# Kernel optimization log

Hardware: AMD Instinct MI355X
Metric: run time of the kernel (lower is better)

The kernel has to match this reference:

```python
import jax, jax.numpy as jnp
import numpy as np

N, E, F_IN, H, HEADS, L, DEPTH = 10000, 160000, 128, 64, 8, 6, 3
M = HEADS * H  # 512, fractal transform width
OUT_DIM = 64
EPS = 1e-5
CHAOS = 0.1


def _ln(x, g, b):
    mu = x.mean(-1, keepdims=True)
    var = x.var(-1, keepdims=True)
    return (x - mu) / jnp.sqrt(var + EPS) * g + b


def _ln_plain(x):
    mu = x.mean(-1, keepdims=True)
    var = x.var(-1, keepdims=True)
    return (x - mu) / jnp.sqrt(var + EPS)


def setup_inputs() -> dict:
    key = jax.random.key(0)
    ks = iter(jax.random.split(key, 64))
    r = lambda *s: jax.random.normal(next(ks), s, jnp.float32) * 0.05
    return dict(
        x=jax.random.normal(next(ks), (N, F_IN), jnp.float32),
        edge_index=jax.random.randint(next(ks), (2, E), 0, N),
        enc_W=r(F_IN, H), enc_b=jnp.zeros((H,)), enc_g=jnp.ones((H,)), enc_beta=jnp.zeros((H,)),
        chaos_memory=r(1, H),
        tW0=r(L, H, M), tb0=jnp.zeros((L, M)), tg0=jnp.ones((L, M)), tbeta0=jnp.zeros((L, M)),
        tW1=r(L, M, M), tb1=jnp.zeros((L, M)), tg1=jnp.ones((L, M)), tbeta1=jnp.zeros((L, M)),
        tW2=r(L, M, M), tb2=jnp.zeros((L, M)), tg2=jnp.ones((L, M)), tbeta2=jnp.zeros((L, M)),
        att=r(L, HEADS, 2 * H),
        evo_W1=r(H, 2 * H), evo_b1=jnp.zeros((2 * H,)),
        evo_W2=r(2 * H, H), evo_b2=jnp.zeros((H,)),
        dec_state_W=r(H, 1), dec_state_b=jnp.zeros((1,)),
        dec_imp_W=r(H, 1), dec_imp_b=jnp.zeros((1,)),
        dec_chaos_W=r(H, 1), dec_chaos_b=jnp.zeros((1,)),
        dec_evo_W=r(H, OUT_DIM), dec_evo_b=jnp.zeros((OUT_DIM,)),
    )


def reference(x, edge_index, enc_W, enc_b, enc_g, enc_beta, chaos_memory,
              tW0, tb0, tg0, tbeta0, tW1, tb1, tg1, tbeta1, tW2, tb2, tg2, tbeta2,
              att, evo_W1, evo_b1, evo_W2, evo_b2,
              dec_state_W, dec_state_b, dec_imp_W, dec_imp_b,
              dec_chaos_W, dec_chaos_b, dec_evo_W, dec_evo_b):
    src, dst = edge_index[0], edge_index[1]  # j -> i, aggregate at dst
    nkey = jax.random.key(42)

    # encoder (dropout inactive in eval)
    h = jax.nn.relu(_ln(x @ enc_W + enc_b, enc_g, enc_beta))
    h = h + chaos_memory * CHAOS  # [1,H] broadcast

    residuals = []
    for i in range(L):
        cf = CHAOS * (1.0 + 0.1 * i)
        h_prev = h
        # fractal transform stack: pre-noise features are averaged
        Ws = [(tW0[i], tb0[i], tg0[i], tbeta0[i]),
              (tW1[i], tb1[i], tg1[i], tbeta1[i]),
              (tW2[i], tb2[i], tg2[i], tbeta2[i])]
        cur = h
        feats = 0.0
        for d, (W, b, g, be) in enumerate(Ws):
            cur = jax.nn.relu(_ln(cur @ W + b, g, be))
            feats = feats + cur
            noise = jax.random.normal(jax.random.fold_in(nkey, i * 10 + d), cur.shape, cur.dtype)
            cur = cur + noise * cf  # chaotic perturbation feeds next depth only
        hm = (feats / DEPTH).reshape(-1, HEADS, H)  # [N, heads, out]
        # GAT-style edge attention: alpha_e = <[x_i||x_j], att>
        a_i = jnp.einsum('nhc,hc->nh', hm, att[i][:, :H])
        a_j = jnp.einsum('nhc,hc->nh', hm, att[i][:, H:])
        alpha = jax.nn.leaky_relu(a_i[dst] + a_j[src], 0.2)  # [E, heads]
        # segment softmax over incoming edges of each dst node
        amax = jax.ops.segment_max(alpha, dst, num_segments=N)
        ex = jnp.exp(alpha - amax[dst])
        denom = jax.ops.segment_sum(ex, dst, num_segments=N)
        w = ex / denom[dst]  # [E, heads]
        msg = hm[src] * w[:, :, None]  # [E, heads, out]
        agg = jax.ops.segment_sum(msg, dst, num_segments=N)  # [N, heads, out]
        h_new = agg.mean(axis=1)  # head-mean -> [N, H]
        gate = jax.nn.sigmoid(jnp.tanh(jax.nn.relu(h_new @ evo_W1 + evo_b1) @ evo_W2 + evo_b2))
        h = gate * h_new + (1.0 - gate) * h_prev
        residuals.append(h)
        h = _ln_plain(h)  # F.layer_norm without affine
    h_multi = sum(residuals) / L
    # batch is None -> decoders applied per-node on h_multi
    state = h_multi @ dec_state_W + dec_state_b
    importance = h_multi @ dec_imp_W + dec_imp_b
    chaos = h_multi @ dec_chaos_W + dec_chaos_b
    evolution = h_multi @ dec_evo_W + dec_evo_b
    return state, importance, chaos, evolution, h_multi
```

## Files before the change

### kernel.cpp

```cpp
#include <hip/hip_runtime.h>
#include <cstdint>
#include <cstddef>

#define NN 10000
#define EE 160000
#define F_IN 128
#define HH 64
#define HEADS 8
#define LL 6
#define MM 512
#define OUT_DIM 64
#define EPSF 1e-5f
#define ROWS 16
#define NB 625

typedef unsigned short ushort;
typedef __attribute__((ext_vector_type(8))) short bf16x8;
typedef __attribute__((ext_vector_type(8))) unsigned short ushort8;
typedef __attribute__((ext_vector_type(4))) float f32x4;

union U8 { ushort8 u; bf16x8 b; };

struct U2 { uint32_t a, b; };

__host__ __device__ constexpr uint32_t rotl32(uint32_t x, uint32_t d) {
  return (x << d) | (x >> (32u - d));
}

__host__ __device__ constexpr U2 threefry2x32(uint32_t k1, uint32_t k2, uint32_t x0, uint32_t x1) {
  uint32_t ks2 = k1 ^ k2 ^ 0x1BD11BDAu;
  x0 += k1; x1 += k2;
  x0 += x1; x1 = rotl32(x1, 13); x1 ^= x0;
  x0 += x1; x1 = rotl32(x1, 15); x1 ^= x0;
  x0 += x1; x1 = rotl32(x1, 26); x1 ^= x0;
  x0 += x1; x1 = rotl32(x1, 6);  x1 ^= x0;
  x0 += k2; x1 += ks2 + 1u;
  x0 += x1; x1 = rotl32(x1, 17); x1 ^= x0;
  x0 += x1; x1 = rotl32(x1, 29); x1 ^= x0;
  x0 += x1; x1 = rotl32(x1, 16); x1 ^= x0;
  x0 += x1; x1 = rotl32(x1, 24); x1 ^= x0;
  x0 += ks2; x1 += k1 + 2u;
  x0 += x1; x1 = rotl32(x1, 13); x1 ^= x0;
  x0 += x1; x1 = rotl32(x1, 15); x1 ^= x0;
  x0 += x1; x1 = rotl32(x1, 26); x1 ^= x0;
  x0 += x1; x1 = rotl32(x1, 6);  x1 ^= x0;
  x0 += k1; x1 += k2 + 3u;
  x0 += x1; x1 = rotl32(x1, 17); x1 ^= x0;
  x0 += x1; x1 = rotl32(x1, 29); x1 ^= x0;
  x0 += x1; x1 = rotl32(x1, 16); x1 ^= x0;
  x0 += x1; x1 = rotl32(x1, 24); x1 ^= x0;
  x0 += k2; x1 += ks2 + 4u;
  x0 += x1; x1 = rotl32(x1, 13); x1 ^= x0;
  x0 += x1; x1 = rotl32(x1, 15); x1 ^= x0;
  x0 += x1; x1 = rotl32(x1, 26); x1 ^= x0;
  x0 += x1; x1 = rotl32(x1, 6);  x1 ^= x0;
  x0 += ks2; x1 += k1 + 5u;
  return U2{x0, x1};
}

__host__ __device__ constexpr U2 foldKey(uint32_t data) {
  return threefry2x32(0u, 42u, 0u, data);
}

__device__ inline float erfinv_f32(float x) {
  float w = -log1pf(-x * x);
  float p;
  if (w < 5.0f) {
    w -= 2.5f;
    p = 2.81022636e-08f;
    p = fmaf(p, w, 3.43273939e-07f);
    p = fmaf(p, w, -3.5233877e-06f);
    p = fmaf(p, w, -4.39150654e-06f);
    p = fmaf(p, w, 0.00021858087f);
    p = fmaf(p, w, -0.00125372503f);
    p = fmaf(p, w, -0.00417768164f);
    p = fmaf(p, w, 0.246640727f);
    p = fmaf(p, w, 1.50140941f);
  } else {
    w = sqrtf(w) - 3.0f;
    p = -0.000200214257f;
    p = fmaf(p, w, 0.000100950558f);
    p = fmaf(p, w, 0.00134934322f);
    p = fmaf(p, w, -0.00367342844f);
    p = fmaf(p, w, 0.00573950773f);
    p = fmaf(p, w, -0.0076224613f);
    p = fmaf(p, w, 0.00943887047f);
    p = fmaf(p, w, 1.00167406f);
    p = fmaf(p, w, 2.83297682f);
  }
  return p * x;
}

__device__ inline float jax_normal(uint32_t k1, uint32_t k2, uint32_t idx) {
  U2 r = threefry2x32(k1, k2, 0u, idx);
  uint32_t bits = r.a ^ r.b;
  uint32_t fb = (bits >> 9) | 0x3f800000u;
  float f = __uint_as_float(fb) - 1.0f;
  const float lo = -0.99999994f;
  float u = f * 2.0f + lo;
  u = fmaxf(lo, u);
  return 1.41421356f * erfinv_f32(u);
}

__device__ inline float waveSum(float v) {
  v += __shfl_xor(v, 32, 64);
  v += __shfl_xor(v, 16, 64);
  v += __shfl_xor(v, 8, 64);
  v += __shfl_xor(v, 4, 64);
  v += __shfl_xor(v, 2, 64);
  v += __shfl_xor(v, 1, 64);
  return v;
}
__device__ inline float waveMax(float v) {
  v = fmaxf(v, __shfl_xor(v, 32, 64));
  v = fmaxf(v, __shfl_xor(v, 16, 64));
  v = fmaxf(v, __shfl_xor(v, 8, 64));
  v = fmaxf(v, __shfl_xor(v, 4, 64));
  v = fmaxf(v, __shfl_xor(v, 2, 64));
  v = fmaxf(v, __shfl_xor(v, 1, 64));
  return v;
}

__device__ inline ushort bf16rn(float x) {
  uint32_t u = __float_as_uint(x);
  uint32_t r = (u + 0x7fffu + ((u >> 16) & 1u)) >> 16;
  return (ushort)r;
}
__device__ inline float bf16tof(ushort h) {
  return __uint_as_float(((uint32_t)h) << 16);
}


__global__ __launch_bounds__(256) void noise_kernel(
    ushort* __restrict__ nz, uint32_t k0a, uint32_t k0b, uint32_t k1a, uint32_t k1b, float cfac) {
  const int GRP = NN * MM / 8;
  int gsz = gridDim.x * blockDim.x;
  for (int g = blockIdx.x * blockDim.x + threadIdx.x; g < 2 * GRP; g += gsz) {
    int slot = (g >= GRP) ? 1 : 0;
    uint32_t ka = slot ? k1a : k0a, kb = slot ? k1b : k0b;
    uint32_t base = (uint32_t)(g - slot * GRP) * 8u;
    ushort out[8];
    #pragma unroll 1
    for (int e = 0; e < 8; ++e)
      out[e] = bf16rn(jax_normal(ka, kb, base + e) * cfac);
    *(ushort8*)(nz + (size_t)slot * NN * MM + base) = *(const ushort8*)out;
  }
}

__global__ __launch_bounds__(64) void encoder_kernel(
    const float* __restrict__ x, const float* __restrict__ W, const float* __restrict__ b,
    const float* __restrict__ g, const float* __restrict__ be, const float* __restrict__ cm,
    float* __restrict__ h, ushort* __restrict__ hHi, ushort* __restrict__ hLo) {
  __shared__ float xs[F_IN];
  int n = blockIdx.x, l = threadIdx.x;
  xs[l]      = x[(size_t)n * F_IN + l];
  xs[l + 64] = x[(size_t)n * F_IN + 64 + l];
  __syncthreads();
  float acc = b[l];
  #pragma unroll 8
  for (int k = 0; k < F_IN; k++) acc = fmaf(xs[k], W[k * HH + l], acc);
  float mu = waveSum(acc) * (1.0f / 64.0f);
  float d = acc - mu;
  float var = waveSum(d * d) * (1.0f / 64.0f);
  float y = fmaf(d / sqrtf(var + EPSF), g[l], be[l]);
  y = fmaxf(y, 0.0f);
  float hv = fmaf(cm[l], 0.1f, y);
  h[(size_t)n * HH + l] = hv;
  ushort hi = bf16rn(hv);
  size_t oi = ((size_t)(l >> 5) * NN + n) * 32 + (l & 31);
  hHi[oi] = hi;
  hLo[oi] = bf16rn(hv - bf16tof(hi));
}

__global__ __launch_bounds__(256) void wconv(
    const float* __restrict__ W, ushort* __restrict__ oh, ushort* __restrict__ ol, int K) {
  __shared__ ushort Th[64][40], Tl[64][40];
  int kt = blockIdx.x;
  int m0 = blockIdx.y * 64;
  int lay = blockIdx.z;
  const float* Wl = W + (size_t)lay * K * MM;
  ushort* ohl = oh + (size_t)lay * K * MM;
  ushort* oll = ol + (size_t)lay * K * MM;
  int t = threadIdx.x;
  #pragma unroll
  for (int p = 0; p < 2; ++p) {
    int li = p * 256 + t;
    int k = li >> 4, mg = (li & 15) * 4;
    float4 v = *(const float4*)(Wl + (size_t)(kt * 32 + k) * MM + m0 + mg);
    float vv[4] = {v.x, v.y, v.z, v.w};
    #pragma unroll
    for (int q = 0; q < 4; ++q) {
      ushort hi = bf16rn(vv[q]);
      Th[mg + q][k] = hi;
      Tl[mg + q][k] = bf16rn(vv[q] - bf16tof(hi));
    }
  }
  __syncthreads();
  #pragma unroll
  for (int p = 0; p < 2; ++p) {
    int li = p * 256 + t;
    int plane = li >> 8;
    int rem = li & 255;
    int m = rem >> 2, kh = (rem & 3) * 8;
    size_t go = ((size_t)kt * MM + m0 + m) * 32 + kh;
    if (plane == 0) *(ushort8*)(ohl + go) = *(const ushort8*)&Th[m][kh];
    else            *(ushort8*)(oll + go) = *(const ushort8*)&Tl[m][kh];
  }
}

__device__ __forceinline__ void do_gemm(
    const uint32_t (&yA)[16][ROWS][36],
    const ushort* __restrict__ Wh, const ushort* __restrict__ Wl,
    int nkt, int colBase, int lr, int kh, f32x4 (&acc)[4]) {
  U8 bh[4], bl[4];
  size_t baseoff = (size_t)(colBase + lr) * 32 + kh;
  #pragma unroll
  for (int cf = 0; cf < 4; ++cf) {
    bh[cf].u = *(const ushort8*)(Wh + baseoff + (size_t)cf * 512);
    bl[cf].u = *(const ushort8*)(Wl + baseoff + (size_t)cf * 512);
  }
  for (int kt = 0; kt < nkt; ++kt) {
    int ktn = (kt + 1 < nkt) ? kt + 1 : kt;
    size_t noff = (size_t)ktn * (MM * 32) + baseoff;
    U8 nbh[4], nbl[4];
    #pragma unroll
    for (int cf = 0; cf < 4; ++cf) {
      nbh[cf].u = *(const ushort8*)(Wh + noff + (size_t)cf * 512);
      nbl[cf].u = *(const ushort8*)(Wl + noff + (size_t)cf * 512);
    }
    const uint32_t* p = &yA[kt][lr][kh];
    uint32_t q[8];
    *(uint4*)&q[0] = *(const uint4*)p;
    *(uint4*)&q[4] = *(const uint4*)(p + 4);
    U8 hu, lu;
    #pragma unroll
    for (int e = 0; e < 8; ++e) {
      hu.u[e] = (ushort)(q[e] & 0xffffu);
      lu.u[e] = (ushort)(q[e] >> 16);
    }
    #pragma unroll
    for (int cf = 0; cf < 4; ++cf) {
      acc[cf] = __builtin_amdgcn_mfma_f32_16x16x32_bf16(hu.b, bh[cf].b, acc[cf], 0, 0, 0);
      acc[cf] = __builtin_amdgcn_mfma_f32_16x16x32_bf16(hu.b, bl[cf].b, acc[cf], 0, 0, 0);
      acc[cf] = __builtin_amdgcn_mfma_f32_16x16x32_bf16(lu.b, bh[cf].b, acc[cf], 0, 0, 0);
    }
    #pragma unroll
    for (int cf = 0; cf < 4; ++cf) { bh[cf] = nbh[cf]; bl[cf] = nbl[cf]; }
  }
}

__device__ __forceinline__ void epi(
    f32x4 (&acc)[4], f32x4 (&fa)[4],
    const float* __restrict__ bias, const float* __restrict__ g, const float* __restrict__ be,
    float (&redS)[8][ROWS], float (&redQ)[8][ROWS],
    uint32_t (&yA)[16][ROWS][36],
    int w, int lr, int r4, int n0,
    bool first, bool writeY, const ushort (&nzr)[16]) {
  int colBase = w * 64;
  float bv[4], gv[4], bev[4];
  #pragma unroll
  for (int cq = 0; cq < 4; ++cq) {
    int col = colBase + cq * 16 + lr;
    bv[cq] = bias[col]; gv[cq] = g[col]; bev[cq] = be[col];
  }
  #pragma unroll
  for (int cq = 0; cq < 4; ++cq) acc[cq] += bv[cq];
  float s[4], q[4];
  #pragma unroll
  for (int j = 0; j < 4; ++j) {
    float sv = 0.f, qv = 0.f;
    #pragma unroll
    for (int cq = 0; cq < 4; ++cq) {
      float a = acc[cq][j];
      sv += a; qv = fmaf(a, a, qv);
    }
    s[j] = sv; q[j] = qv;
  }
  #pragma unroll
  for (int d = 8; d >= 1; d >>= 1)
    #pragma unroll
    for (int u = 0; u < 4; ++u) {
      s[u] += __shfl_xor(s[u], d, 64);
      q[u] += __shfl_xor(q[u], d, 64);
    }
  if (lr == 0) {
    #pragma unroll
    for (int j = 0; j < 4; ++j) {
      redS[w][r4 * 4 + j] = s[j];
      redQ[w][r4 * 4 + j] = q[j];
    }
  }
  __syncthreads();
  float mu[4], inv[4];
  #pragma unroll
  for (int j = 0; j < 4; ++j) {
    int row = r4 * 4 + j;
    float S = 0.f, Q = 0.f;
    #pragma unroll
    for (int ww = 0; ww < 8; ++ww) { S += redS[ww][row]; Q += redQ[ww][row]; }
    float m = S * (1.0f / 512.0f);
    float v = fmaxf(Q * (1.0f / 512.0f) - m * m, 0.0f);
    mu[j] = m;
    inv[j] = 1.0f / sqrtf(v + EPSF);
  }
  #pragma unroll
  for (int cq = 0; cq < 4; ++cq) {
    int c = colBase + cq * 16 + lr;
    #pragma unroll
    for (int j = 0; j < 4; ++j) {
      int row = r4 * 4 + j;
      float o = fmaxf(fmaf((acc[cq][j] - mu[j]) * inv[j], gv[cq], bev[cq]), 0.0f);
      if (first) fa[cq][j] = o; else fa[cq][j] += o;
      if (writeY) {
        float y = o + bf16tof(nzr[cq * 4 + j]);
        ushort hi = bf16rn(y);
        ushort lo = bf16rn(y - bf16tof(hi));
        yA[c >> 5][row][c & 31] = (uint32_t)hi | ((uint32_t)lo << 16);
      }
    }
  }
}

__global__ __launch_bounds__(512) void layer_fused(
    const ushort* __restrict__ hHi, const ushort* __restrict__ hLo,
    const ushort* __restrict__ W0h, const ushort* __restrict__ W0l,
    const ushort* __restrict__ W1h, const ushort* __restrict__ W1l,
    const ushort* __restrict__ W2h, const ushort* __restrict__ W2l,
    const float* __restrict__ b0, const float* __restrict__ g0, const float* __restrict__ be0,
    const float* __restrict__ b1, const float* __restrict__ g1, const float* __restrict__ be1,
    const float* __restrict__ b2, const float* __restrict__ g2, const float* __restrict__ be2,
    const float* __restrict__ attL, const ushort* __restrict__ nz,
    uint32_t* __restrict__ featsPk, float* __restrict__ ai, float* __restrict__ aj) {
  __shared__ __align__(16) uint32_t yA[16][ROWS][36];
  __shared__ float redS[8][ROWS], redQ[8][ROWS];
  int t = threadIdx.x, w = t >> 6, lane = t & 63;
  int lr = lane & 15, r4 = lane >> 4, kh = r4 * 8;
  int n0 = blockIdx.x * ROWS, colBase = w * 64;

  ushort nzr[16];
  #pragma unroll
  for (int cq = 0; cq < 4; ++cq)
    #pragma unroll
    for (int j = 0; j < 4; ++j)
      nzr[cq * 4 + j] = nz[(size_t)(n0 + r4 * 4 + j) * MM + colBase + cq * 16 + lr];

  #pragma unroll
  for (int p = 0; p < 2; ++p) {
    int li = p * 512 + t;
    int r = li >> 6, c = li & 63;
    int kt = c >> 5, kk = c & 31;
    int n = n0 + r;
    ushort hv = hHi[((size_t)kt * NN + n) * 32 + kk];
    ushort lv = hLo[((size_t)kt * NN + n) * 32 + kk];
    yA[kt][r][kk] = (uint32_t)hv | ((uint32_t)lv << 16);
  }
  __syncthreads();

  f32x4 acc[4], fa[4];
  #pragma unroll
  for (int j = 0; j < 4; j++) acc[j] = (f32x4){0.f, 0.f, 0.f, 0.f};

  do_gemm(yA, W0h, W0l, 2, colBase, lr, kh, acc);
  epi(acc, fa, b0, g0, be0, redS, redQ, yA, w, lr, r4, n0, true, true, nzr);
  __syncthreads();

  #pragma unroll
  for (int cq = 0; cq < 4; ++cq)
    #pragma unroll
    for (int j = 0; j < 4; ++j)
      nzr[cq * 4 + j] = nz[(size_t)NN * MM + (size_t)(n0 + r4 * 4 + j) * MM + colBase + cq * 16 + lr];

  #pragma unroll
  for (int j = 0; j < 4; j++) acc[j] = (f32x4){0.f, 0.f, 0.f, 0.f};
  do_gemm(yA, W1h, W1l, 16, colBase, lr, kh, acc);
  epi(acc, fa, b1, g1, be1, redS, redQ, yA, w, lr, r4, n0, false, true, nzr);
  __syncthreads();

  #pragma unroll
  for (int j = 0; j < 4; j++) acc[j] = (f32x4){0.f, 0.f, 0.f, 0.f};
  do_gemm(yA, W2h, W2l, 16, colBase, lr, kh, acc);
  epi(acc, fa, b2, g2, be2, redS, redQ, yA, w, lr, r4, n0, false, false, nzr);

  const float inv3 = 1.0f / 3.0f;
  float atI[4], atJ[4];
  #pragma unroll
  for (int cq = 0; cq < 4; ++cq) {
    atI[cq] = attL[w * 128 + cq * 16 + lr];
    atJ[cq] = attL[w * 128 + 64 + cq * 16 + lr];
  }
  ushort* fs = (ushort*)yA;
  #pragma unroll
  for (int j = 0; j < 4; ++j) {
    float si = 0.f, sj = 0.f;
    #pragma unroll
    for (int cq = 0; cq < 4; ++cq) {
      float f0 = fa[cq][j];
      si = fmaf(f0, atI[cq], si); sj = fmaf(f0, atJ[cq], sj);
    }
    #pragma unroll
    for (int d = 8; d >= 1; d >>= 1) {
      si += __shfl_xor(si, d, 64); sj += __shfl_xor(sj, d, 64);
    }
    int row = r4 * 4 + j;
    int n = n0 + row;
    if (lr == 0) {
      ai[n * 8 + w] = si * inv3;
      aj[n * 8 + w] = sj * inv3;
    }
    #pragma unroll
    for (int cq = 0; cq < 4; ++cq)
      fs[row * 520 + colBase + cq * 16 + lr] = bf16rn(fa[cq][j] * inv3);
  }
  __syncthreads();
  #pragma unroll
  for (int p = 0; p < 8; ++p) {
    int li = p * 512 + t;
    int row = li >> 8, m = li & 255;
    int c0 = (m >> 6) * 128 + (m & 63);
    uint32_t v = (uint32_t)fs[row * 520 + c0] | ((uint32_t)fs[row * 520 + c0 + 64] << 16);
    featsPk[(size_t)(n0 + row) * 256 + m] = v;
  }
}

__global__ __launch_bounds__(256) void csr_histo(const int* __restrict__ dst, int* __restrict__ deg) {
  int e = blockIdx.x * blockDim.x + threadIdx.x;
  if (e < EE) atomicAdd(&deg[dst[e]], 1);
}

__global__ __launch_bounds__(256) void csr_scan(const int* __restrict__ deg, int* __restrict__ offs) {
  __shared__ int part[256];
  int t = threadIdx.x;
  const int chunk = (NN + 255) / 256;
  int start = t * chunk;
  int s = 0;
  for (int j = 0; j < chunk; j++) { int i = start + j; if (i < NN) s += deg[i]; }
  part[t] = s; __syncthreads();
  for (int d = 1; d < 256; d <<= 1) {
    int v = (t >= d) ? part[t - d] : 0;
    __syncthreads();
    part[t] += v;
    __syncthreads();
  }
  int run = (t == 0) ? 0 : part[t - 1];
  for (int j = 0; j < chunk; j++) {
    int i = start + j;
    if (i < NN) { offs[i] = run; run += deg[i]; }
  }
  if (t == 0) offs[NN] = EE;
}

__global__ __launch_bounds__(256) void csr_fill(const int* __restrict__ src, const int* __restrict__ dst,
                                                int* __restrict__ pos, int* __restrict__ csrc) {
  int e = blockIdx.x * blockDim.x + threadIdx.x;
  if (e >= EE) return;
  int d = dst[e];
  int slot = atomicAdd(&pos[d], 1);
  csrc[slot] = src[e];
}

__global__ __launch_bounds__(256) void gat_fused(
    const int* __restrict__ offs, const int* __restrict__ csrc,
    const float* __restrict__ ai, const float* __restrict__ aj,
    const uint32_t* __restrict__ featsPk,
    const float* __restrict__ W1, const float* __restrict__ b1,
    const float* __restrict__ W2, const float* __restrict__ b2,
    float* __restrict__ h, float* __restrict__ resid,
    ushort* __restrict__ hHi, ushort* __restrict__ hLo) {
  int n = blockIdx.x, t = threadIdx.x, wid = t >> 6, l = t & 63;
  int e0 = offs[n], e1 = offs[n + 1];
  int hA = wid * 2;
  float2 aiv = *(const float2*)&ai[n * HEADS + hA];

  float m0 = -1e30f, m1 = -1e30f, s0 = 0.f, s1 = 0.f;
  for (int c = e0; c < e1; c += 64) {
    int idx = c + l;
    bool act = idx < e1;
    float a0 = -1e30f, a1 = -1e30f;
    if (act) {
      int sv = csrc[idx];
      float2 ajv = *(const float2*)&aj[sv * HEADS + hA];
      a0 = aiv.x + ajv.x; a0 = (a0 >= 0.f) ? a0 : 0.2f * a0;
      a1 = aiv.y + ajv.y; a1 = (a1 >= 0.f) ? a1 : 0.2f * a1;
    }
    float cm0 = waveMax(a0), cm1 = waveMax(a1);
    float mn0 = fmaxf(m0, cm0), mn1 = fmaxf(m1, cm1);
    float e0v = act ? expf(a0 - mn0) : 0.f;
    float e1v = act ? expf(a1 - mn1) : 0.f;
    float sc0 = (m0 > -1e29f) ? expf(m0 - mn0) : 0.f;
    float sc1 = (m1 > -1e29f) ? expf(m1 - mn1) : 0.f;
    s0 = s0 * sc0 + waveSum(e0v);
    s1 = s1 * sc1 + waveSum(e1v);
    m0 = mn0; m1 = mn1;
  }
  float is0 = (s0 > 0.f) ? 1.0f / s0 : 0.f;
  float is1 = (s1 > 0.f) ? 1.0f / s1 : 0.f;

  __shared__ int sSrc[64];
  __shared__ float sEx[8][64];
  float acc0 = 0.f, acc1 = 0.f;
  for (int c = e0; c < e1; c += 64) {
    int idx = c + l;
    bool act = idx < e1;
    if (act) {
      int sv = csrc[idx];
      if (wid == 0) sSrc[l] = sv;
      float2 ajv = *(const float2*)&aj[sv * HEADS + hA];
      float a0 = aiv.x + ajv.x; a0 = (a0 >= 0.f) ? a0 : 0.2f * a0;
      float a1 = aiv.y + ajv.y; a1 = (a1 >= 0.f) ? a1 : 0.2f * a1;
      sEx[hA][l]     = expf(a0 - m0) * is0;
      sEx[hA + 1][l] = expf(a1 - m1) * is1;
    }
    __syncthreads();
    int cnt = min(64, e1 - c);
    for (int j = 0; j < cnt; ++j) {
      uint32_t pv = featsPk[(size_t)sSrc[j] * 256 + wid * 64 + l];
      acc0 = fmaf(bf16tof((ushort)(pv & 0xffffu)), sEx[hA][j], acc0);
      acc1 = fmaf(bf16tof((ushort)(pv >> 16)),     sEx[hA + 1][j], acc1);
    }
    __syncthreads();
  }

  __shared__ float hacc[4][64];
  hacc[wid][l] = acc0 + acc1;
  __syncthreads();
  __shared__ float hn[64];
  __shared__ float z[128];
  if (t < 64) hn[t] = (hacc[0][t] + hacc[1][t] + hacc[2][t] + hacc[3][t]) * 0.125f;
  __syncthreads();
  if (t < 128) {
    float zz = b1[t];
    #pragma unroll 8
    for (int k = 0; k < 64; k++) zz = fmaf(hn[k], W1[k * 128 + t], zz);
    z[t] = fmaxf(zz, 0.f);
  }
  __syncthreads();
  if (t < 64) {
    float y = b2[t];
    #pragma unroll 8
    for (int k = 0; k < 128; k++) y = fmaf(z[k], W2[k * 64 + t], y);
    float gate = 1.0f / (1.0f + expf(-tanhf(y)));
    float hp = h[(size_t)n * HH + t];
    float hb = gate * hn[t] + (1.0f - gate) * hp;
    resid[(size_t)n * HH + t] += hb;
    float mu = waveSum(hb) * (1.0f / 64.0f);
    float dd = hb - mu;
    float var = waveSum(dd * dd) * (1.0f / 64.0f);
    float hv = dd / sqrtf(var + EPSF);
    h[(size_t)n * HH + t] = hv;
    ushort hi = bf16rn(hv);
    size_t oi = ((size_t)(t >> 5) * NN + n) * 32 + (t & 31);
    hHi[oi] = hi;
    hLo[oi] = bf16rn(hv - bf16tof(hi));
  }
}

__global__ __launch_bounds__(64) void decoder_kernel(
    const float* __restrict__ resid,
    const float* __restrict__ dsW, const float* __restrict__ dsb,
    const float* __restrict__ diW, const float* __restrict__ dib,
    const float* __restrict__ dcW, const float* __restrict__ dcb,
    const float* __restrict__ deW, const float* __restrict__ deb,
    float* __restrict__ out) {
  __shared__ float hm[64];
  int n = blockIdx.x, l = threadIdx.x;
  float v = resid[(size_t)n * HH + l] * (1.0f / 6.0f);
  hm[l] = v;
  float s1 = waveSum(v * dsW[l]);
  float s2 = waveSum(v * diW[l]);
  float s3 = waveSum(v * dcW[l]);
  if (l == 0) {
    out[n]          = s1 + dsb[0];
    out[NN + n]     = s2 + dib[0];
    out[2 * NN + n] = s3 + dcb[0];
  }
  __syncthreads();
  float e = deb[l];
  #pragma unroll 8
  for (int k = 0; k < 64; k++) e = fmaf(hm[k], deW[k * OUT_DIM + l], e);
  out[3 * NN + (size_t)n * OUT_DIM + l] = e;
  out[3 * NN + (size_t)NN * OUT_DIM + (size_t)n * HH + l] = v;
}

extern "C" void kernel_launch(void* const* d_in, const int* in_sizes, int n_in,
                              void* d_out, int out_size, void* d_ws, size_t ws_size,
                              hipStream_t stream) {
  const float* x        = (const float*)d_in[0];
  const int*   ei       = (const int*)d_in[1];
  const float* enc_W    = (const float*)d_in[2];
  const float* enc_b    = (const float*)d_in[3];
  const float* enc_g    = (const float*)d_in[4];
  const float* enc_beta = (const float*)d_in[5];
  const float* cm       = (const float*)d_in[6];
  const float* tW0 = (const float*)d_in[7];  const float* tb0 = (const float*)d_in[8];
  const float* tg0 = (const float*)d_in[9];  const float* tbe0 = (const float*)d_in[10];
  const float* tW1 = (const float*)d_in[11]; const float* tb1 = (const float*)d_in[12];
  const float* tg1 = (const float*)d_in[13]; const float* tbe1 = (const float*)d_in[14];
  const float* tW2 = (const float*)d_in[15]; const float* tb2 = (const float*)d_in[16];
  const float* tg2 = (const float*)d_in[17]; const float* tbe2 = (const float*)d_in[18];
  const float* att = (const float*)d_in[19];
  const float* evo_W1 = (const float*)d_in[20]; const float* evo_b1 = (const float*)d_in[21];
  const float* evo_W2 = (const float*)d_in[22]; const float* evo_b2 = (const float*)d_in[23];
  const float* dsW = (const float*)d_in[24]; const float* dsb = (const float*)d_in[25];
  const float* diW = (const float*)d_in[26]; const float* dib = (const float*)d_in[27];
  const float* dcW = (const float*)d_in[28]; const float* dcb = (const float*)d_in[29];
  const float* deW = (const float*)d_in[30]; const float* deb = (const float*)d_in[31];
  float* out = (float*)d_out;

  const int* src = ei;
  const int* dst = ei + EE;

  float* ws = (float*)d_ws;
  size_t o = 0;
  float* h     = ws + o; o += (size_t)NN * HH;
  float* resid = ws + o; o += (size_t)NN * HH;
  float* ai    = ws + o; o += (size_t)NN * HEADS;
  float* aj    = ws + o; o += (size_t)NN * HEADS;
  int* deg  = (int*)(ws + o); o += NN;
  int* offs = (int*)(ws + o); o += NN + 2;
  int* pos  = (int*)(ws + o); o += NN;
  int* csrc = (int*)(ws + o); o += EE;
  o = (o + 3) & ~(size_t)3;
  uint32_t* featsPk = (uint32_t*)(ws + o); o += (size_t)NN * 256;
  ushort* us = (ushort*)(ws + o);
  size_t uo = 0;
  ushort* W0h = us + uo; uo += (size_t)LL * HH * MM;
  ushort* W0l = us + uo; uo += (size_t)LL * HH * MM;
  ushort* W1h = us + uo; uo += (size_t)LL * MM * MM;
  ushort* W1l = us + uo; uo += (size_t)LL * MM * MM;
  ushort* W2h = us + uo; uo += (size_t)LL * MM * MM;
  ushort* W2l = us + uo; uo += (size_t)LL * MM * MM;
  ushort* hHi = us + uo; uo += (size_t)NN * HH;
  ushort* hLo = us + uo; uo += (size_t)NN * HH;
  ushort* nz  = us + uo; uo += (size_t)2 * NN * MM;
  (void)ws_size; (void)n_in; (void)in_sizes; (void)out_size;

  wconv<<<dim3(2, 8, 6), 256, 0, stream>>>(tW0, W0h, W0l, HH);
  wconv<<<dim3(16, 8, 6), 256, 0, stream>>>(tW1, W1h, W1l, MM);
  wconv<<<dim3(16, 8, 6), 256, 0, stream>>>(tW2, W2h, W2l, MM);

  hipMemsetAsync(deg, 0, (size_t)NN * sizeof(int), stream);
  csr_histo<<<(EE + 255) / 256, 256, 0, stream>>>(dst, deg);
  csr_scan<<<1, 256, 0, stream>>>(deg, offs);
  hipMemcpyAsync(pos, offs, (size_t)NN * sizeof(int), hipMemcpyDeviceToDevice, stream);
  csr_fill<<<(EE + 255) / 256, 256, 0, stream>>>(src, dst, pos, csrc);

  encoder_kernel<<<NN, 64, 0, stream>>>(x, enc_W, enc_b, enc_g, enc_beta, cm, h, hHi, hLo);
  hipMemsetAsync(resid, 0, (size_t)NN * HH * sizeof(float), stream);

  for (int i = 0; i < LL; ++i) {
    float cfac = (float)(0.1 * (1.0 + 0.1 * (double)i));
    U2 fk0 = foldKey((uint32_t)(i * 10 + 0));
    U2 fk1 = foldKey((uint32_t)(i * 10 + 1));

    noise_kernel<<<2048, 256, 0, stream>>>(nz, fk0.a, fk0.b, fk1.a, fk1.b, cfac);

    layer_fused<<<NB, 512, 0, stream>>>(
        hHi, hLo,
        W0h + (size_t)i * HH * MM, W0l + (size_t)i * HH * MM,
        W1h + (size_t)i * MM * MM, W1l + (size_t)i * MM * MM,
        W2h + (size_t)i * MM * MM, W2l + (size_t)i * MM * MM,
        tb0 + (size_t)i * MM, tg0 + (size_t)i * MM, tbe0 + (size_t)i * MM,
        tb1 + (size_t)i * MM, tg1 + (size_t)i * MM, tbe1 + (size_t)i * MM,
        tb2 + (size_t)i * MM, tg2 + (size_t)i * MM, tbe2 + (size_t)i * MM,
        att + (size_t)i * HEADS * 2 * HH, nz,
        featsPk, ai, aj);

    gat_fused<<<NN, 256, 0, stream>>>(offs, csrc, ai, aj, featsPk,
        evo_W1, evo_b1, evo_W2, evo_b2, h, resid, hHi, hLo);
  }

  decoder_kernel<<<NN, 64, 0, stream>>>(resid, dsW, dsb, diW, dib, dcW, dcb, deW, deb, out);
}
```

Before: 1.497 ms.

## Double rows per block in fused transform GEMM and unroll GAT gather loop

The fused fractal-transform kernel now processes 32 node rows per block instead of 16. Each wave loads a weight fragment once and reuses it for two row fragments, which halves weight traffic per row. The software prefetch of the next weight tile is dropped, bounds guards are added for the partial last block, and a 4-waves occupancy hint is set. Separately, the GAT neighbor gather loop is unrolled by four so several independent feature loads are in flight at once. The risks are higher register pressure, fewer blocks (313) across the CUs, and exposed weight-load latency now that prefetch is gone.

New measurement: 1.517 ms. Within noise of the previous version (+1.3%).

```diff
diff --git a/kernel.cpp b/kernel.cpp
--- a/kernel.cpp
+++ b/kernel.cpp
@@ -11,8 +11,8 @@
 #define MM 512
 #define OUT_DIM 64
 #define EPSF 1e-5f
-#define ROWS 16
-#define NB 625
+#define ROWS 32
+#define NB2 313
 
 typedef unsigned short ushort;
 typedef __attribute__((ext_vector_type(8))) short bf16x8;
@@ -211,51 +211,44 @@
 __device__ __forceinline__ void do_gemm(
     const uint32_t (&yA)[16][ROWS][36],
     const ushort* __restrict__ Wh, const ushort* __restrict__ Wl,
-    int nkt, int colBase, int lr, int kh, f32x4 (&acc)[4]) {
-  U8 bh[4], bl[4];
-  size_t baseoff = (size_t)(colBase + lr) * 32 + kh;
-  #pragma unroll
-  for (int cf = 0; cf < 4; ++cf) {
-    bh[cf].u = *(const ushort8*)(Wh + baseoff + (size_t)cf * 512);
-    bl[cf].u = *(const ushort8*)(Wl + baseoff + (size_t)cf * 512);
-  }
+    int nkt, int colBase, int lr, int kh, f32x4 (&acc)[2][4]) {
   for (int kt = 0; kt < nkt; ++kt) {
-    int ktn = (kt + 1 < nkt) ? kt + 1 : kt;
-    size_t noff = (size_t)ktn * (MM * 32) + baseoff;
-    U8 nbh[4], nbl[4];
+    U8 bh[4], bl[4];
+    size_t off0 = (size_t)kt * (MM * 32) + (size_t)(colBase + lr) * 32 + kh;
     #pragma unroll
     for (int cf = 0; cf < 4; ++cf) {
-      nbh[cf].u = *(const ushort8*)(Wh + noff + (size_t)cf * 512);
-      nbl[cf].u = *(const ushort8*)(Wl + noff + (size_t)cf * 512);
-    }
-    const uint32_t* p = &yA[kt][lr][kh];
-    uint32_t q[8];
-    *(uint4*)&q[0] = *(const uint4*)p;
-    *(uint4*)&q[4] = *(const uint4*)(p + 4);
-    U8 hu, lu;
-    #pragma unroll
-    for (int e = 0; e < 8; ++e) {
-      hu.u[e] = (ushort)(q[e] & 0xffffu);
-      lu.u[e] = (ushort)(q[e] >> 16);
-    }
-    #pragma unroll
-    for (int cf = 0; cf < 4; ++cf) {
-      acc[cf] = __builtin_amdgcn_mfma_f32_16x16x32_bf16(hu.b, bh[cf].b, acc[cf], 0, 0, 0);
-      acc[cf] = __builtin_amdgcn_mfma_f32_16x16x32_bf16(hu.b, bl[cf].b, acc[cf], 0, 0, 0);
-      acc[cf] = __builtin_amdgcn_mfma_f32_16x16x32_bf16(lu.b, bh[cf].b, acc[cf], 0, 0, 0);
-    }
-    #pragma unroll
-    for (int cf = 0; cf < 4; ++cf) { bh[cf] = nbh[cf]; bl[cf] = nbl[cf]; }
+      bh[cf].u = *(const ushort8*)(Wh + off0 + (size_t)cf * 512);
+      bl[cf].u = *(const ushort8*)(Wl + off0 + (size_t)cf * 512);
+    }
+    #pragma unroll
+    for (int rf = 0; rf < 2; ++rf) {
+      const uint32_t* p = &yA[kt][rf * 16 + lr][kh];
+      uint32_t q[8];
+      *(uint4*)&q[0] = *(const uint4*)p;
+      *(uint4*)&q[4] = *(const uint4*)(p + 4);
+      U8 hu, lu;
+      #pragma unroll
+      for (int e = 0; e < 8; ++e) {
+        hu.u[e] = (ushort)(q[e] & 0xffffu);
+        lu.u[e] = (ushort)(q[e] >> 16);
+      }
+      #pragma unroll
+      for (int cf = 0; cf < 4; ++cf) {
+        acc[rf][cf] = __builtin_amdgcn_mfma_f32_16x16x32_bf16(hu.b, bh[cf].b, acc[rf][cf], 0, 0, 0);
+        acc[rf][cf] = __builtin_amdgcn_mfma_f32_16x16x32_bf16(hu.b, bl[cf].b, acc[rf][cf], 0, 0, 0);
+        acc[rf][cf] = __builtin_amdgcn_mfma_f32_16x16x32_bf16(lu.b, bh[cf].b, acc[rf][cf], 0, 0, 0);
+      }
+    }
   }
 }
 
 __device__ __forceinline__ void epi(
-    f32x4 (&acc)[4], f32x4 (&fa)[4],
+    f32x4 (&acc)[2][4], f32x4 (&fa)[2][4],
     const float* __restrict__ bias, const float* __restrict__ g, const float* __restrict__ be,
     float (&redS)[8][ROWS], float (&redQ)[8][ROWS],
     uint32_t (&yA)[16][ROWS][36],
-    int w, int lr, int r4, int n0,
-    bool first, bool writeY, const ushort (&nzr)[16]) {
+    int w, int lr, int r4,
+    bool first, bool writeY, const ushort (&nzr)[32]) {
   int colBase = w * 64;
   float bv[4], gv[4], bev[4];
   #pragma unroll
@@ -264,64 +257,74 @@
     bv[cq] = bias[col]; gv[cq] = g[col]; bev[cq] = be[col];
   }
   #pragma unroll
-  for (int cq = 0; cq < 4; ++cq) acc[cq] += bv[cq];
-  float s[4], q[4];
-  #pragma unroll
-  for (int j = 0; j < 4; ++j) {
-    float sv = 0.f, qv = 0.f;
-    #pragma unroll
-    for (int cq = 0; cq < 4; ++cq) {
-      float a = acc[cq][j];
-      sv += a; qv = fmaf(a, a, qv);
-    }
-    s[j] = sv; q[j] = qv;
-  }
+  for (int rf = 0; rf < 2; ++rf)
+    #pragma unroll
+    for (int cq = 0; cq < 4; ++cq) acc[rf][cq] += bv[cq];
+  float s[8], q[8];
+  #pragma unroll
+  for (int rf = 0; rf < 2; ++rf)
+    #pragma unroll
+    for (int j = 0; j < 4; ++j) {
+      float sv = 0.f, qv = 0.f;
+      #pragma unroll
+      for (int cq = 0; cq < 4; ++cq) {
+        float a = acc[rf][cq][j];
+        sv += a; qv = fmaf(a, a, qv);
+      }
+      s[rf * 4 + j] = sv; q[rf * 4 + j] = qv;
+    }
   #pragma unroll
   for (int d = 8; d >= 1; d >>= 1)
     #pragma unroll
-    for (int u = 0; u < 4; ++u) {
+    for (int u = 0; u < 8; ++u) {
       s[u] += __shfl_xor(s[u], d, 64);
       q[u] += __shfl_xor(q[u], d, 64);
     }
   if (lr == 0) {
     #pragma unroll
+    for (int rf = 0; rf < 2; ++rf)
+      #pragma unroll
+      for (int j = 0; j < 4; ++j) {
+        redS[w][rf * 16 + r4 * 4 + j] = s[rf * 4 + j];
+        redQ[w][rf * 16 + r4 * 4 + j] = q[rf * 4 + j];
+      }
+  }
+  __syncthreads();
+  float mu[8], inv[8];
+  #pragma unroll
+  for (int rf = 0; rf < 2; ++rf)
+    #pragma unroll
     for (int j = 0; j < 4; ++j) {
-      redS[w][r4 * 4 + j] = s[j];
-      redQ[w][r4 * 4 + j] = q[j];
-    }
-  }
-  __syncthreads();
-  float mu[4], inv[4];
-  #pragma unroll
-  for (int j = 0; j < 4; ++j) {
-    int row = r4 * 4 + j;
-    float S = 0.f, Q = 0.f;
-    #pragma unroll
-    for (int ww = 0; ww < 8; ++ww) { S += redS[ww][row]; Q += redQ[ww][row]; }
-    float m = S * (1.0f / 512.0f);
-    float v = fmaxf(Q * (1.0f / 512.0f) - m * m, 0.0f);
-    mu[j] = m;
-    inv[j] = 1.0f / sqrtf(v + EPSF);
-  }
-  #pragma unroll
-  for (int cq = 0; cq < 4; ++cq) {
-    int c = colBase + cq * 16 + lr;
-    #pragma unroll
-    for (int j = 0; j < 4; ++j) {
-      int row = r4 * 4 + j;
-      float o = fmaxf(fmaf((acc[cq][j] - mu[j]) * inv[j], gv[cq], bev[cq]), 0.0f);
-      if (first) fa[cq][j] = o; else fa[cq][j] += o;
-      if (writeY) {
-        float y = o + bf16tof(nzr[cq * 4 + j]);
-        ushort hi = bf16rn(y);
-        ushort lo = bf16rn(y - bf16tof(hi));
-        yA[c >> 5][row][c & 31] = (uint32_t)hi | ((uint32_t)lo << 16);
-      }
-    }
-  }
-}
-
-__global__ __launch_bounds__(512) void layer_fused(
+      int row = rf * 16 + r4 * 4 + j;
+      float S = 0.f, Q = 0.f;
+      #pragma unroll
+      for (int ww = 0; ww < 8; ++ww) { S += redS[ww][row]; Q += redQ[ww][row]; }
+      float m = S * (1.0f / 512.0f);
+      float v = fmaxf(Q * (1.0f / 512.0f) - m * m, 0.0f);
+      mu[rf * 4 + j] = m;
+      inv[rf * 4 + j] = 1.0f / sqrtf(v + EPSF);
+    }
+  #pragma unroll
+  for (int rf = 0; rf < 2; ++rf)
+    #pragma unroll
+    for (int cq = 0; cq < 4; ++cq) {
+      int c = colBase + cq * 16 + lr;
+      #pragma unroll
+      for (int j = 0; j < 4; ++j) {
+        int row = rf * 16 + r4 * 4 + j;
+        float o = fmaxf(fmaf((acc[rf][cq][j] - mu[rf * 4 + j]) * inv[rf * 4 + j], gv[cq], bev[cq]), 0.0f);
+        if (first) fa[rf][cq][j] = o; else fa[rf][cq][j] += o;
+        if (writeY) {
+          float y = o + bf16tof(nzr[rf * 16 + cq * 4 + j]);
+          ushort hi = bf16rn(y);
+          ushort lo = bf16rn(y - bf16tof(hi));
+          yA[c >> 5][row][c & 31] = (uint32_t)hi | ((uint32_t)lo << 16);
+        }
+      }
+    }
+}
+
+__global__ __launch_bounds__(512, 4) void layer_fused(
     const ushort* __restrict__ hHi, const ushort* __restrict__ hLo,
     const ushort* __restrict__ W0h, const ushort* __restrict__ W0l,
     const ushort* __restrict__ W1h, const ushort* __restrict__ W1l,
@@ -337,49 +340,66 @@
   int lr = lane & 15, r4 = lane >> 4, kh = r4 * 8;
   int n0 = blockIdx.x * ROWS, colBase = w * 64;
 
-  ushort nzr[16];
-  #pragma unroll
-  for (int cq = 0; cq < 4; ++cq)
-    #pragma unroll
-    for (int j = 0; j < 4; ++j)
-      nzr[cq * 4 + j] = nz[(size_t)(n0 + r4 * 4 + j) * MM + colBase + cq * 16 + lr];
-
-  #pragma unroll
-  for (int p = 0; p < 2; ++p) {
+  ushort nzr[32];
+  #pragma unroll
+  for (int rf = 0; rf < 2; ++rf)
+    #pragma unroll
+    for (int cq = 0; cq < 4; ++cq)
+      #pragma unroll
+      for (int j = 0; j < 4; ++j) {
+        int nn = n0 + rf * 16 + r4 * 4 + j; if (nn >= NN) nn = NN - 1;
+        nzr[rf * 16 + cq * 4 + j] = nz[(size_t)nn * MM + colBase + cq * 16 + lr];
+      }
+
+  #pragma unroll
+  for (int p = 0; p < 4; ++p) {
     int li = p * 512 + t;
     int r = li >> 6, c = li & 63;
     int kt = c >> 5, kk = c & 31;
     int n = n0 + r;
-    ushort hv = hHi[((size_t)kt * NN + n) * 32 + kk];
-    ushort lv = hLo[((size_t)kt * NN + n) * 32 + kk];
+    ushort hv = 0, lv = 0;
+    if (n < NN) {
+      hv = hHi[((size_t)kt * NN + n) * 32 + kk];
+      lv = hLo[((size_t)kt * NN + n) * 32 + kk];
+    }
     yA[kt][r][kk] = (uint32_t)hv | ((uint32_t)lv << 16);
   }
   __syncthreads();
 
-  f32x4 acc[4], fa[4];
-  #pragma unroll
-  for (int j = 0; j < 4; j++) acc[j] = (f32x4){0.f, 0.f, 0.f, 0.f};
+  f32x4 acc[2][4], fa[2][4];
+  #pragma unroll
+  for (int rf = 0; rf < 2; ++rf)
+    #pragma unroll
+    for (int j = 0; j < 4; j++) acc[rf][j] = (f32x4){0.f, 0.f, 0.f, 0.f};
 
   do_gemm(yA, W0h, W0l, 2, colBase, lr, kh, acc);
-  epi(acc, fa, b0, g0, be0, redS, redQ, yA, w, lr, r4, n0, true, true, nzr);
-  __syncthreads();
-
-  #pragma unroll
-  for (int cq = 0; cq < 4; ++cq)
-    #pragma unroll
-    for (int j = 0; j < 4; ++j)
-      nzr[cq * 4 + j] = nz[(size_t)NN * MM + (size_t)(n0 + r4 * 4 + j) * MM + colBase + cq * 16 + lr];
-
-  #pragma unroll
-  for (int j = 0; j < 4; j++) acc[j] = (f32x4){0.f, 0.f, 0.f, 0.f};
+  epi(acc, fa, b0, g0, be0, redS, redQ, yA, w, lr, r4, true, true, nzr);
+  __syncthreads();
+
+  #pragma unroll
+  for (int rf = 0; rf < 2; ++rf)
+    #pragma unroll
+    for (int cq = 0; cq < 4; ++cq)
+      #pragma unroll
+      for (int j = 0; j < 4; ++j) {
+        int nn = n0 + rf * 16 + r4 * 4 + j; if (nn >= NN) nn = NN - 1;
+        nzr[rf * 16 + cq * 4 + j] = nz[(size_t)NN * MM + (size_t)nn * MM + colBase + cq * 16 + lr];
+      }
+
+  #pragma unroll
+  for (int rf = 0; rf < 2; ++rf)
+    #pragma unroll
+    for (int j = 0; j < 4; j++) acc[rf][j] = (f32x4){0.f, 0.f, 0.f, 0.f};
   do_gemm(yA, W1h, W1l, 16, colBase, lr, kh, acc);
-  epi(acc, fa, b1, g1, be1, redS, redQ, yA, w, lr, r4, n0, false, true, nzr);
-  __syncthreads();
-
-  #pragma unroll
-  for (int j = 0; j < 4; j++) acc[j] = (f32x4){0.f, 0.f, 0.f, 0.f};
+  epi(acc, fa, b1, g1, be1, redS, redQ, yA, w, lr, r4, false, true, nzr);
+  __syncthreads();
+
+  #pragma unroll
+  for (int rf = 0; rf < 2; ++rf)
+    #pragma unroll
+    for (int j = 0; j < 4; j++) acc[rf][j] = (f32x4){0.f, 0.f, 0.f, 0.f};
   do_gemm(yA, W2h, W2l, 16, colBase, lr, kh, acc);
-  epi(acc, fa, b2, g2, be2, redS, redQ, yA, w, lr, r4, n0, false, false, nzr);
+  epi(acc, fa, b2, g2, be2, redS, redQ, yA, w, lr, r4, false, false, nzr);
 
   const float inv3 = 1.0f / 3.0f;
   float atI[4], atJ[4];
@@ -390,35 +410,40 @@
   }
   ushort* fs = (ushort*)yA;
   #pragma unroll
-  for (int j = 0; j < 4; ++j) {
-    float si = 0.f, sj = 0.f;
-    #pragma unroll
-    for (int cq = 0; cq < 4; ++cq) {
-      float f0 = fa[cq][j];
-      si = fmaf(f0, atI[cq], si); sj = fmaf(f0, atJ[cq], sj);
-    }
-    #pragma unroll
-    for (int d = 8; d >= 1; d >>= 1) {
-      si += __shfl_xor(si, d, 64); sj += __shfl_xor(sj, d, 64);
-    }
-    int row = r4 * 4 + j;
-    int n = n0 + row;
-    if (lr == 0) {
-      ai[n * 8 + w] = si * inv3;
-      aj[n * 8 + w] = sj * inv3;
-    }
-    #pragma unroll
-    for (int cq = 0; cq < 4; ++cq)
-      fs[row * 520 + colBase + cq * 16 + lr] = bf16rn(fa[cq][j] * inv3);
-  }
-  __syncthreads();
-  #pragma unroll
-  for (int p = 0; p < 8; ++p) {
+  for (int rf = 0; rf < 2; ++rf)
+    #pragma unroll
+    for (int j = 0; j < 4; ++j) {
+      float si = 0.f, sj = 0.f;
+      #pragma unroll
+      for (int cq = 0; cq < 4; ++cq) {
+        float f0 = fa[rf][cq][j];
+        si = fmaf(f0, atI[cq], si); sj = fmaf(f0, atJ[cq], sj);
+      }
+      #pragma unroll
+      for (int d = 8; d >= 1; d >>= 1) {
+        si += __shfl_xor(si, d, 64); sj += __shfl_xor(sj, d, 64);
+      }
+      int row = rf * 16 + r4 * 4 + j;
+      int n = n0 + row;
+      if (lr == 0 && n < NN) {
+        ai[n * 8 + w] = si * inv3;
+        aj[n * 8 + w] = sj * inv3;
+      }
+      #pragma unroll
+      for (int cq = 0; cq < 4; ++cq)
+        fs[row * 520 + colBase + cq * 16 + lr] = bf16rn(fa[rf][cq][j] * inv3);
+    }
+  __syncthreads();
+  #pragma unroll
+  for (int p = 0; p < 16; ++p) {
     int li = p * 512 + t;
     int row = li >> 8, m = li & 255;
-    int c0 = (m >> 6) * 128 + (m & 63);
-    uint32_t v = (uint32_t)fs[row * 520 + c0] | ((uint32_t)fs[row * 520 + c0 + 64] << 16);
-    featsPk[(size_t)(n0 + row) * 256 + m] = v;
+    int n = n0 + row;
+    if (n < NN) {
+      int c0 = (m >> 6) * 128 + (m & 63);
+      uint32_t v = (uint32_t)fs[row * 520 + c0] | ((uint32_t)fs[row * 520 + c0 + 64] << 16);
+      featsPk[(size_t)n * 256 + m] = v;
+    }
   }
 }
 
@@ -498,6 +523,7 @@
   __shared__ int sSrc[64];
   __shared__ float sEx[8][64];
   float acc0 = 0.f, acc1 = 0.f;
+  const size_t lnoff = (size_t)wid * 64 + l;
   for (int c = e0; c < e1; c += 64) {
     int idx = c + l;
     bool act = idx < e1;
@@ -512,8 +538,23 @@
     }
     __syncthreads();
     int cnt = min(64, e1 - c);
-    for (int j = 0; j < cnt; ++j) {
-      uint32_t pv = featsPk[(size_t)sSrc[j] * 256 + wid * 64 + l];
+    int j = 0;
+    for (; j + 4 <= cnt; j += 4) {
+      uint32_t p0 = featsPk[(size_t)sSrc[j + 0] * 256 + lnoff];
+      uint32_t p1 = featsPk[(size_t)sSrc[j + 1] * 256 + lnoff];
+      uint32_t p2 = featsPk[(size_t)sSrc[j + 2] * 256 + lnoff];
+      uint32_t p3 = featsPk[(size_t)sSrc[j + 3] * 256 + lnoff];
+      acc0 = fmaf(bf16tof((ushort)(p0 & 0xffffu)), sEx[hA][j + 0], acc0);
+      acc1 = fmaf(bf16tof((ushort)(p0 >> 16)),     sEx[hA + 1][j + 0], acc1);
+      acc0 = fmaf(bf16tof((ushort)(p1 & 0xffffu)), sEx[hA][j + 1], acc0);
+      acc1 = fmaf(bf16tof((ushort)(p1 >> 16)),     sEx[hA + 1][j + 1], acc1);
+      acc0 = fmaf(bf16tof((ushort)(p2 & 0xffffu)), sEx[hA][j + 2], acc0);
+      acc1 = fmaf(bf16tof((ushort)(p2 >> 16)),     sEx[hA + 1][j + 2], acc1);
+      acc0 = fmaf(bf16tof((ushort)(p3 & 0xffffu)), sEx[hA][j + 3], acc0);
+      acc1 = fmaf(bf16tof((ushort)(p3 >> 16)),     sEx[hA + 1][j + 3], acc1);
+    }
+    for (; j < cnt; ++j) {
+      uint32_t pv = featsPk[(size_t)sSrc[j] * 256 + lnoff];
       acc0 = fmaf(bf16tof((ushort)(pv & 0xffffu)), sEx[hA][j], acc0);
       acc1 = fmaf(bf16tof((ushort)(pv >> 16)),     sEx[hA + 1][j], acc1);
     }
@@ -654,7 +695,7 @@
 
     noise_kernel<<<2048, 256, 0, stream>>>(nz, fk0.a, fk0.b, fk1.a, fk1.b, cfac);
 
-    layer_fused<<<NB, 512, 0, stream>>>(
+    layer_fused<<<NB2, 512, 0, stream>>>(
         hHi, hLo,
         W0h + (size_t)i * HH * MM, W0l + (size_t)i * HH * MM,
         W1h + (size_t)i * MM * MM, W1l + (size_t)i * MM * MM,
```
